# Kernel tuning notes

Measured on AMD Instinct MI355X. Metric: run time of the kernel, lower is better.

The kernel has to match this reference:

```python
import jax, jax.numpy as jnp
import numpy as np

N = 4096      # num_nodes
U = 64        # num_units
IN = 2        # input_dim
DIM = U + IN  # 66
H = 4         # attention heads
ALPHA = 0.2   # leaky slope inside attention scores
SLOPE = 0.01  # nn.LeakyReLU() default for subnet activations
NEG_INF = -9e15


def setup_inputs() -> dict:
    key = jax.random.key(0)
    ks = jax.random.split(key, 20)
    def gn(k, shape, fan):
        return jax.random.normal(k, shape, dtype=jnp.float32) / np.float32(np.sqrt(fan))
    adj = jax.random.randint(ks[2], (N, N), 0, 2, dtype=jnp.int32)
    adj = jnp.maximum(adj, jnp.eye(N, dtype=jnp.int32))  # ensure self-loops
    return {
        "inputs": jax.random.normal(ks[0], (1, N * IN), dtype=jnp.float32),
        "hx": jax.random.normal(ks[1], (1, N, U), dtype=jnp.float32),
        "adj": adj,
        "m1_W": gn(ks[3], (H, DIM, DIM), DIM),
        "m1_a1": gn(ks[4], (H, DIM), DIM),
        "m1_a2": gn(ks[5], (H, DIM), DIM),
        "m1_Wout": gn(ks[6], (H * DIM, DIM), H * DIM),
        "m1_ao1": gn(ks[7], (DIM,), DIM),
        "m1_ao2": gn(ks[8], (DIM,), DIM),
        "m2_W": gn(ks[9], (H, DIM, DIM), DIM),
        "m2_a1": gn(ks[10], (H, DIM), DIM),
        "m2_a2": gn(ks[11], (H, DIM), DIM),
        "m2_Wout": gn(ks[12], (H * DIM, DIM), H * DIM),
        "m2_ao1": gn(ks[13], (DIM,), DIM),
        "m2_ao2": gn(ks[14], (DIM,), DIM),
        "g1_W": gn(ks[15], (DIM, 2 * U), DIM),
        "g1_b": jnp.zeros((2 * U,), dtype=jnp.float32),
        "g2_W": gn(ks[16], (DIM, U), DIM),
        "g2_b": jnp.zeros((U,), dtype=jnp.float32),
    }


def gat_layer(x, W, a1, a2, mask):
    # x: [N,Fin], W: [Fin,Fout], a1/a2: [Fout], mask: [N,N] bool
    h = x @ W                                   # [N,Fout]
    f1 = h @ a1                                 # [N] source term
    f2 = h @ a2                                 # [N] target term
    e = jax.nn.leaky_relu(f1[:, None] + f2[None, :], ALPHA)  # [N,N]
    e = jnp.where(mask, e, NEG_INF)
    attn = jax.nn.softmax(e, axis=-1)
    return attn @ h                             # [N,Fout]


def subnet(x, W, a1, a2, Wout, ao1, ao2, mask):
    # multi-head GAT, concat heads, activation, output GAT layer, activation
    heads = jax.vmap(gat_layer, in_axes=(None, 0, 0, 0, None))(x, W, a1, a2, mask)  # [H,N,DIM]
    hcat = jnp.transpose(heads, (1, 0, 2)).reshape(x.shape[0], -1)                   # [N,H*DIM]
    hcat = jax.nn.leaky_relu(hcat, SLOPE)
    out = gat_layer(hcat, Wout, ao1, ao2, mask)                                      # [N,DIM]
    return jax.nn.leaky_relu(out, SLOPE)


def reference(inputs, hx, adj, m1_W, m1_a1, m1_a2, m1_Wout, m1_ao1, m1_ao2,
              m2_W, m2_a1, m2_a2, m2_Wout, m2_ao1, m2_ao2,
              g1_W, g1_b, g2_W, g2_b):
    mask = adj > 0
    xi = inputs.reshape(N, IN)
    xh = hx.reshape(N, U)
    # _GAT1: concat(inputs, hx) -> GATSubNet1 -> linear -> sigmoid -> split r,u
    x1 = jnp.concatenate([xi, xh], axis=-1)                 # [N,DIM]
    g1 = subnet(x1, m1_W, m1_a1, m1_a2, m1_Wout, m1_ao1, m1_ao2, mask)
    value = jax.nn.sigmoid(g1 @ g1_W + g1_b)                # [N,2U]
    r, u = value[:, :U], value[:, U:]
    # _GAT2: concat(inputs, r*hx) -> GATSubNet2 -> linear -> tanh
    x2 = jnp.concatenate([xi, r * xh], axis=-1)             # [N,DIM]
    g2 = subnet(x2, m2_W, m2_a1, m2_a2, m2_Wout, m2_ao1, m2_ao2, mask)
    c = jnp.tanh(g2 @ g2_W + g2_b)                          # [N,U]
    new_state = u * xh + (1.0 - u) * c
    return new_state.reshape(1, N, U)
```

## Files before the change

### kernel.cpp

```cpp
#include <hip/hip_runtime.h>
#include <hip/hip_bf16.h>

constexpr int kN = 4096;
constexpr int kDim = 66;
constexpr int kH = 4;
constexpr int kU = 64;
constexpr float kAlpha = 0.2f;
constexpr float kSlope = 0.01f;
constexpr float kLog2e = 1.44269504f;

typedef _Float16 half8 __attribute__((ext_vector_type(8)));
typedef _Float16 half2t __attribute__((ext_vector_type(2)));
typedef __attribute__((ext_vector_type(4))) float floatx4;

__device__ inline unsigned int fkey(float f){
  unsigned int u = __float_as_uint(f);
  return (u & 0x80000000u) ? ~u : (u | 0x80000000u);
}
__device__ inline float funkey(unsigned int k){
  unsigned int u = (k & 0x80000000u) ? (k ^ 0x80000000u) : ~k;
  return __uint_as_float(u);
}

__device__ __forceinline__ void gld_lds16(const void* g, void* l){
  __builtin_amdgcn_global_load_lds((const __attribute__((address_space(1))) unsigned int*)g,
                                   (__attribute__((address_space(3))) unsigned int*)l, 16, 0, 0);
}

__global__ void setup_k(const int* __restrict__ adj, unsigned long long* __restrict__ packed,
                        const float* __restrict__ in2, const float* __restrict__ hx,
                        _Float16* __restrict__ x1b, _Float16* __restrict__ x2b,
                        const float* __restrict__ m1W, const float* __restrict__ m1a1, const float* __restrict__ m1a2,
                        const float* __restrict__ m1Wo, const float* __restrict__ m1ao1, const float* __restrict__ m1ao2,
                        const float* __restrict__ m2W, const float* __restrict__ m2a1, const float* __restrict__ m2a2,
                        const float* __restrict__ m2Wo, const float* __restrict__ m2ao1, const float* __restrict__ m2ao2,
                        const float* __restrict__ g1W, const float* __restrict__ g1b,
                        const float* __restrict__ g2W, const float* __restrict__ g2b,
                        _Float16* __restrict__ B1t, _Float16* __restrict__ B1t2,
                        _Float16* __restrict__ B2t, _Float16* __restrict__ B2t2,
                        _Float16* __restrict__ Bgt, _Float16* __restrict__ Bft,
                        unsigned int* __restrict__ fmaxbuf){
  int bb = blockIdx.x, t = threadIdx.x;
  if (bb < 16384){
    int gid = bb * 256 + t;
    unsigned long long m = __ballot(adj[gid] != 0);
    if ((t & 63) == 0) packed[gid >> 6] = m;
    return;
  }
  if (bb < 16384 + 1024){
    int i = (bb - 16384) * 4 + (t >> 6);
    int c = t & 63;
    x1b[(size_t)i * 96 + 2 + c] = (_Float16)hx[(size_t)i * kU + c];
    if (c < 2){
      _Float16 xv = (_Float16)in2[i * 2 + c];
      x1b[(size_t)i * 96 + c] = xv;
      x2b[(size_t)i * 96 + c] = xv;
    }
    if (c < 30){
      x1b[(size_t)i * 96 + 66 + c] = (_Float16)0.f;
      x2b[(size_t)i * 96 + 66 + c] = (_Float16)0.f;
    }
    return;
  }
  int b = bb - (16384 + 1024);
  if (b < 8){
    int m = b & 3;
    const float* W  = (b < 4 ? m1W  : m2W)  + (size_t)m * kDim * kDim;
    const float* a1 = (b < 4 ? m1a1 : m2a1) + m * kDim;
    const float* a2 = (b < 4 ? m1a2 : m2a2) + m * kDim;
    _Float16* Bo = (b < 4 ? B1t : B1t2) + (size_t)m * 80 * 96;
    __shared__ float Ws[kDim * kDim];
    __shared__ float wa1s[kDim], wa2s[kDim];
    for (int z = t; z < kDim * kDim; z += 256) Ws[z] = W[z];
    __syncthreads();
    if (t < kDim){
      float s1 = 0.f, s2 = 0.f;
      for (int d = 0; d < kDim; d++){ float wv = Ws[t * kDim + d]; s1 += wv * a1[d]; s2 += wv * a2[d]; }
      wa1s[t] = s1; wa2s[t] = s2;
    }
    __syncthreads();
    for (int z = t; z < 80 * 96; z += 256){
      int nn = z / 96, k = z % 96;
      float val = 0.f;
      if (k < kDim){
        if (nn < kDim) val = Ws[k * kDim + nn];
        else if (nn == 66) val = wa1s[k];
        else if (nn == 67) val = wa2s[k];
      }
      Bo[z] = (_Float16)val;
    }
  } else if (b < 10){
    const float* Wo  = (b == 8 ? m1Wo  : m2Wo);
    const float* ao1 = (b == 8 ? m1ao1 : m2ao1);
    const float* ao2 = (b == 8 ? m1ao2 : m2ao2);
    _Float16* Bo = (b == 8 ? B2t : B2t2);
    __shared__ float wo1s[264], wo2s[264];
    for (int k = t; k < 264; k += 256){
      float s1 = 0.f, s2 = 0.f;
      for (int d = 0; d < kDim; d++){ float wv = Wo[(size_t)k * kDim + d]; s1 += wv * ao1[d]; s2 += wv * ao2[d]; }
      wo1s[k] = s1; wo2s[k] = s2;
    }
    __syncthreads();
    for (int z = t; z < 80 * 288; z += 256){
      int nn = z / 288, k = z % 288;
      int h = k / 72, c = k - h * 72;
      float val = 0.f;
      if (c < 66){
        int kk = h * 66 + c;
        if (nn < kDim) val = Wo[(size_t)kk * kDim + nn];
        else if (nn == 66) val = wo1s[kk];
        else if (nn == 67) val = wo2s[kk];
      }
      Bo[z] = (_Float16)val;
    }
  } else if (b == 10){
    for (int z = t; z < 128 * 96; z += 256){
      int nn = z / 96, k = z % 96;
      float val = 0.f;
      if (k < kDim) val = g1W[k * 128 + nn];
      else if (k == 66) val = g1b[nn];
      Bgt[z] = (_Float16)val;
    }
  } else {
    if (t < 16) fmaxbuf[t] = 0u;
    for (int z = t; z < 64 * 96; z += 256){
      int nn = z / 96, k = z % 96;
      float val = 0.f;
      if (k < kDim) val = g2W[k * 64 + nn];
      else if (k == 66) val = g2b[nn];
      Bft[z] = (_Float16)val;
    }
  }
}

template<int KSTEPS, int NT, int EPI>
__global__ __launch_bounds__(256) void gemm_k(
    const _Float16* __restrict__ A, const _Float16* __restrict__ Bt,
    void* __restrict__ p0, void* __restrict__ p1, void* __restrict__ p2,
    const float* __restrict__ aux, unsigned int* __restrict__ fmaxp)
{
  constexpr int KP = KSTEPS * 32;
  const int m = blockIdx.y;
  const int i0 = blockIdx.x * 64;
  const int t = threadIdx.x;
  const int w = t >> 6, lane = t & 63, q = lane >> 4, n = lane & 15;
  const int arow = i0 + w * 16 + n;
  const _Float16* Ar = A + (size_t)arow * KP;
  const _Float16* Bm = Bt + (size_t)m * (NT * 16) * KP;
  floatx4 acc[NT];
  #pragma unroll
  for (int v = 0; v < NT; v++) acc[v] = (floatx4){0.f, 0.f, 0.f, 0.f};
  #pragma unroll
  for (int ks = 0; ks < KSTEPS; ks++){
    half8 af = *(const half8*)&Ar[ks * 32 + q * 8];
    #pragma unroll
    for (int nt = 0; nt < NT; nt++){
      half8 bf = *(const half8*)&Bm[(size_t)(nt * 16 + n) * KP + ks * 32 + q * 8];
      acc[nt] = __builtin_amdgcn_mfma_f32_16x16x32_f16(af, bf, acc[nt], 0, 0, 0);
    }
  }
  const int ib = i0 + w * 16 + q * 4;
  if constexpr (EPI == 0){
    _Float16* Ht = (_Float16*)p0 + (size_t)m * 68 * kN;
    float* f1 = (float*)p1 + (size_t)m * kN;
    float* f2 = (float*)p2 + (size_t)m * kN;
    float lm = -3e38f;
    #pragma unroll
    for (int nt = 0; nt < NT; nt++){
      int c = nt * 16 + n;
      if (c < kDim){
        union { _Float16 h[4]; uint2 v; } pk;
        pk.h[0] = (_Float16)acc[nt][0]; pk.h[1] = (_Float16)acc[nt][1];
        pk.h[2] = (_Float16)acc[nt][2]; pk.h[3] = (_Float16)acc[nt][3];
        *(uint2*)&Ht[(size_t)c * kN + ib] = pk.v;
      } else if (c == 66){
        float4 fv; fv.x = acc[nt][0] * kLog2e; fv.y = acc[nt][1] * kLog2e;
        fv.z = acc[nt][2] * kLog2e; fv.w = acc[nt][3] * kLog2e;
        *(float4*)&f1[ib] = fv;
        *(uint2*)&Ht[(size_t)66 * kN + ib] = make_uint2(0x3C003C00u, 0x3C003C00u);
      } else if (c == 67){
        float4 fv; fv.x = acc[nt][0] * kLog2e; fv.y = acc[nt][1] * kLog2e;
        fv.z = acc[nt][2] * kLog2e; fv.w = acc[nt][3] * kLog2e;
        *(float4*)&f2[ib] = fv;
        lm = fmaxf(fmaxf(fv.x, fv.y), fmaxf(fv.z, fv.w));
        *(uint2*)&Ht[(size_t)67 * kN + ib] = make_uint2(0u, 0u);
      }
    }
    lm = fmaxf(lm, __shfl_xor(lm, 16));
    lm = fmaxf(lm, __shfl_xor(lm, 32));
    if (lane == 3) atomicMax(&fmaxp[m], fkey(lm));
  } else if constexpr (EPI == 1){
    float* u = (float*)p0;
    _Float16* x2b = (_Float16*)p1;
    #pragma unroll
    for (int nt = 0; nt < NT; nt++){
      int c = nt * 16 + n;
      #pragma unroll
      for (int r = 0; r < 4; r++){
        float v = 1.f / (1.f + __expf(-acc[nt][r]));
        if (c < 64) x2b[(size_t)(ib + r) * 96 + 2 + c] = (_Float16)(v * aux[(size_t)(ib + r) * kU + c]);
        else        u[(size_t)(ib + r) * kU + (c - 64)] = v;
      }
    }
  } else {
    float* outp = (float*)p0;
    const float* u = (const float*)p1;
    #pragma unroll
    for (int nt = 0; nt < NT; nt++){
      int c = nt * 16 + n;
      #pragma unroll
      for (int r = 0; r < 4; r++){
        float cc = tanhf(acc[nt][r]);
        float uv = u[(size_t)(ib + r) * kU + c];
        outp[(size_t)(ib + r) * kU + c] = uv * aux[(size_t)(ib + r) * kU + c] + (1.f - uv) * cc;
      }
    }
  }
}

template<int JSPLIT>
__global__ __launch_bounds__(256, 4) void attn_mfma_k(
    const _Float16* __restrict__ Ht, const float* __restrict__ f1,
    const float* __restrict__ f2, const unsigned int* __restrict__ fmaxu,
    const unsigned long long* __restrict__ packed,
    _Float16* __restrict__ paccb)
{
  constexpr int JR = kN / JSPLIT;
  constexpr int NCH = JR / 128;
  const int m = blockIdx.y, js = blockIdx.z;
  const int i0 = blockIdx.x * 64;
  const int t = threadIdx.x;
  const int w = t >> 6, lane = t & 63, q = lane >> 4, n = lane & 15;
  const int i = i0 + w * 16 + n;
  const _Float16* Hg = Ht + (size_t)m * 68 * kN;
  const float* f2m = f2 + (size_t)m * kN;
  const float f1v = f1[(size_t)m * kN + i];
  const float fmx = funkey(fmaxu[m]);
  const float t0 = f1v + fmx;
  const float S = fmaxf(t0, kAlpha * t0);
  const float A1f = __builtin_amdgcn_exp2f(t0 - S);
  const float A2f = __builtin_amdgcn_exp2f(kAlpha * t0 - S);
  const half2t a1p = { (_Float16)A1f, (_Float16)A1f };
  const half2t a2p = { (_Float16)A2f, (_Float16)A2f };

  __shared__ __align__(16) _Float16 buf[2][68 * 128];
  __shared__ __align__(16) _Float16 Zro[128];
  __shared__ __align__(16) _Float16 B1h[2][128], B2h[2][128];

  for (int z = t; z < 128; z += 256) Zro[z] = (_Float16)0.f;

  const int r4 = q;
  const int cse = n ^ r4;
  const int cso = cse ^ 4;

  const int jbase = js * JR;
  const unsigned long long* prow = packed + (size_t)i * 64;
  const int jj = (w << 5) | (lane & 31);
  const bool blane = (lane & 32) == 0;

#define STAGE_G(PD, CH) do { \
    const _Float16* gB_ = Hg + jbase + (CH) * 128; \
    _Pragma("unroll") \
    for (int kk_ = 0; kk_ < 5; kk_++){ \
      const int k_ = w + kk_ * 4; \
      if (k_ < 17){ \
        const int row_ = k_ * 4 + r4; \
        const int csw_ = (k_ & 1) ? cso : cse; \
        gld_lds16(gB_ + (size_t)row_ * kN + csw_ * 8, &buf[(PD)][k_ * 512]); \
      } \
    } \
  } while (0)

  floatx4 acc[5];
  #pragma unroll
  for (int v = 0; v < 5; v++) acc[v] = (floatx4){0.f, 0.f, 0.f, 0.f};

  if (blane){
    const float v_ = f2m[jbase + jj] - fmx;
    B1h[0][jj] = (_Float16)__builtin_amdgcn_exp2f(v_);
    B2h[0][jj] = (_Float16)__builtin_amdgcn_exp2f(kAlpha * v_);
  }
  STAGE_G(0, 0);
  __syncthreads();

  int ch = 0;
#define BODY(P) do { \
    const int j0_ = jbase + ch * 128; \
     \
    float f2v_ = 0.f; \
    const bool doB_ = (ch + 1 < NCH) && blane; \
    if (doB_) f2v_ = f2m[j0_ + 128 + jj]; \
    const unsigned long long w0_ = prow[j0_ >> 6]; \
    const unsigned long long w1_ = prow[(j0_ >> 6) + 1]; \
    __builtin_amdgcn_sched_barrier(0); \
    if (ch + 1 < NCH) STAGE_G((P) ^ 1, ch + 1); \
    __builtin_amdgcn_sched_barrier(0); \
    if (doB_){ \
      const float v_ = f2v_ - fmx; \
      B1h[(P) ^ 1][jj] = (_Float16)__builtin_amdgcn_exp2f(v_); \
      B2h[(P) ^ 1][jj] = (_Float16)__builtin_amdgcn_exp2f(kAlpha * v_); \
    } \
    const _Float16* bz_ = (n < 4) ? &buf[(P)][(64 + n) * 128] : Zro; \
    _Pragma("unroll") \
    for (int ks = 0; ks < 4; ks++){ \
      const unsigned long long wsel = (ks < 2) ? w0_ : w1_; \
      const unsigned int bits = (unsigned int)((wsel >> ((ks & 1) * 32 + q * 8)) & 0xffull); \
      union { uint4 v; unsigned int u[4]; } b1v, b2v; \
      b1v.v = *(const uint4*)&B1h[(P)][ks * 32 + q * 8]; \
      b2v.v = *(const uint4*)&B2h[(P)][ks * 32 + q * 8]; \
      union { half8 s; unsigned int u[4]; } af; \
      _Pragma("unroll") \
      for (int e = 0; e < 4; e++){ \
        half2t x1 = __builtin_bit_cast(half2t, b1v.u[e]); \
        half2t x2 = __builtin_bit_cast(half2t, b2v.u[e]); \
        half2t m1 = x1 * a1p; \
        half2t m2 = x2 * a2p; \
        half2t pm = __builtin_elementwise_max(m1, m2); \
        unsigned int mm = (((bits >> (2 * e)) & 1u) ? 0x0000FFFFu : 0u) \
                        | (((bits >> (2 * e + 1)) & 1u) ? 0xFFFF0000u : 0u); \
        af.u[e] = __builtin_bit_cast(unsigned int, pm) & mm; \
      } \
      const int cs_ = ((ks * 4 + q) ^ (n & 7)) * 8; \
      _Pragma("unroll") \
      for (int nt = 0; nt < 4; nt++){ \
        const half8 bf = *(const half8*)&buf[(P)][(nt * 16 + n) * 128 + cs_]; \
        acc[nt] = __builtin_amdgcn_mfma_f32_16x16x32_f16(af.s, bf, acc[nt], 0, 0, 0); \
      } \
      { const half8 bf4 = *(const half8*)&bz_[cs_]; \
        acc[4] = __builtin_amdgcn_mfma_f32_16x16x32_f16(af.s, bf4, acc[4], 0, 0, 0); } \
    } \
    ch++; \
    if (ch < NCH) __syncthreads(); \
  } while (0)

  #pragma unroll 1
  for (int it = 0; it < NCH / 2; it++){
    BODY(0);
    BODY(1);
  }
#undef BODY
#undef STAGE_G

  _Float16* pw = paccb + ((size_t)(m * JSPLIT + js) * kN + (i0 + w * 16)) * 80;
  #pragma unroll
  for (int nt = 0; nt < 5; nt++){
    if (nt < 4 || n < 4){
      #pragma unroll
      for (int r = 0; r < 4; r++)
        pw[(q * 4 + r) * 80 + nt * 16 + n] = (_Float16)acc[nt][r];
    }
  }
}

template<int JSPLIT>
__global__ void combine_k(const _Float16* __restrict__ paccb, _Float16* __restrict__ outb,
                          int ostride, int headoff, int ones_col){
  const int m = blockIdx.y;
  const int t = threadIdx.x;
  const int ri = t >> 2, cg = t & 3;
  const int lane = t & 63;
  const int i = blockIdx.x * 64 + ri;
  const _Float16* pb = paccb + ((size_t)m * JSPLIT * kN + i) * 80;
  float accv[3][8];
  #pragma unroll
  for (int k = 0; k < 3; k++)
    #pragma unroll
    for (int e = 0; e < 8; e++) accv[k][e] = 0.f;
  #pragma unroll
  for (int s = 0; s < JSPLIT; s++){
    const _Float16* ps = pb + (size_t)s * kN * 80;
    #pragma unroll
    for (int k = 0; k < 3; k++){
      const int c = cg + 4 * k;
      if (c < 9){
        union { uint4 v; _Float16 h[8]; } uu;
        uu.v = *(const uint4*)&ps[c * 8];
        #pragma unroll
        for (int e = 0; e < 8; e++) accv[k][e] += (float)uu.h[e];
      }
    }
  }
  float l = accv[2][2];
  l = __shfl(l, lane & ~3, 64);
  const float inv = 1.f / l;
  _Float16* orow = outb + (size_t)i * ostride + m * headoff;
  #pragma unroll
  for (int k = 0; k < 3; k++){
    const int c = cg + 4 * k;
    if (c < 9){
      union { uint4 v; _Float16 h[8]; } uu;
      #pragma unroll
      for (int e = 0; e < 8; e++){
        float v = accv[k][e] * inv;
        v = fmaxf(v, kSlope * v);
        uu.h[e] = (_Float16)v;
      }
      if (c == 8){
        uu.h[2] = (_Float16)(ones_col ? 1.f : 0.f);
        #pragma unroll
        for (int e = 3; e < 8; e++) uu.h[e] = (_Float16)0.f;
      }
      *(uint4*)&orow[c * 8] = uu.v;
    }
  }
}

extern "C" void kernel_launch(void* const* d_in, const int* in_sizes, int n_in,
                              void* d_out, int out_size, void* d_ws, size_t ws_size,
                              hipStream_t stream){
  const float* inputs  = (const float*)d_in[0];
  const float* hx      = (const float*)d_in[1];
  const int*   adj     = (const int*)d_in[2];
  const float* m1_W    = (const float*)d_in[3];
  const float* m1_a1   = (const float*)d_in[4];
  const float* m1_a2   = (const float*)d_in[5];
  const float* m1_Wout = (const float*)d_in[6];
  const float* m1_ao1  = (const float*)d_in[7];
  const float* m1_ao2  = (const float*)d_in[8];
  const float* m2_W    = (const float*)d_in[9];
  const float* m2_a1   = (const float*)d_in[10];
  const float* m2_a2   = (const float*)d_in[11];
  const float* m2_Wout = (const float*)d_in[12];
  const float* m2_ao1  = (const float*)d_in[13];
  const float* m2_ao2  = (const float*)d_in[14];
  const float* g1_W    = (const float*)d_in[15];
  const float* g1_b    = (const float*)d_in[16];
  const float* g2_W    = (const float*)d_in[17];
  const float* g2_b    = (const float*)d_in[18];
  float* out = (float*)d_out;

  char* ws = (char*)d_ws;
  size_t off = 0;
  auto alloc = [&](size_t bytes) -> void* {
    void* p = ws + off;
    off = (off + bytes + 255) & ~(size_t)255;
    return p;
  };
  unsigned long long* packed = (unsigned long long*)alloc((size_t)kN * 64 * 8);
  _Float16* x1b  = (_Float16*)alloc((size_t)kN * 96 * 2);
  _Float16* x2b  = (_Float16*)alloc((size_t)kN * 96 * 2);
  _Float16* Ht   = (_Float16*)alloc((size_t)kH * 68 * kN * 2);
  _Float16* Hto  = (_Float16*)alloc((size_t)68 * kN * 2);
  _Float16* hcatb= (_Float16*)alloc((size_t)kN * 288 * 2);
  _Float16* gb   = (_Float16*)alloc((size_t)kN * 96 * 2);
  _Float16* g2bv = (_Float16*)alloc((size_t)kN * 96 * 2);
  float* f1   = (float*)alloc((size_t)kH * kN * 4);
  float* f2   = (float*)alloc((size_t)kH * kN * 4);
  float* fo1  = (float*)alloc((size_t)kN * 4);
  float* fo2  = (float*)alloc((size_t)kN * 4);
  unsigned int* fmaxbuf = (unsigned int*)alloc(64);
  float* u    = (float*)alloc((size_t)kN * kU * 4);
  _Float16* paccb = (_Float16*)alloc((size_t)16 * kN * 80 * 2);
  _Float16* B1t  = (_Float16*)alloc((size_t)kH * 80 * 96 * 2);
  _Float16* B1t2 = (_Float16*)alloc((size_t)kH * 80 * 96 * 2);
  _Float16* B2t  = (_Float16*)alloc((size_t)80 * 288 * 2);
  _Float16* B2t2 = (_Float16*)alloc((size_t)80 * 288 * 2);
  _Float16* Bgt  = (_Float16*)alloc((size_t)128 * 96 * 2);
  _Float16* Bft  = (_Float16*)alloc((size_t)64 * 96 * 2);
  (void)ws_size; (void)in_sizes; (void)n_in; (void)out_size;

  setup_k<<<16384 + 1024 + 12, 256, 0, stream>>>(adj, packed, inputs, hx, x1b, x2b,
      m1_W, m1_a1, m1_a2, m1_Wout, m1_ao1, m1_ao2,
      m2_W, m2_a1, m2_a2, m2_Wout, m2_ao1, m2_ao2,
      g1_W, g1_b, g2_W, g2_b,
      B1t, B1t2, B2t, B2t2, Bgt, Bft, fmaxbuf);

  gemm_k<3, 5, 0><<<dim3(64, kH), 256, 0, stream>>>(x1b, B1t, Ht, f1, f2, nullptr, fmaxbuf + 0);
  attn_mfma_k<4><<<dim3(64, kH, 4), 256, 0, stream>>>(Ht, f1, f2, fmaxbuf + 0, packed, paccb);
  combine_k<4><<<dim3(64, kH), 256, 0, stream>>>(paccb, hcatb, 288, 72, 0);
  gemm_k<9, 5, 0><<<dim3(64, 1), 256, 0, stream>>>(hcatb, B2t, Hto, fo1, fo2, nullptr, fmaxbuf + 4);
  attn_mfma_k<8><<<dim3(64, 1, 8), 256, 0, stream>>>(Hto, fo1, fo2, fmaxbuf + 4, packed, paccb);
  combine_k<8><<<dim3(64, 1), 256, 0, stream>>>(paccb, gb, 96, 0, 1);
  gemm_k<3, 8, 1><<<dim3(64, 1), 256, 0, stream>>>(gb, Bgt, u, x2b, nullptr, hx, nullptr);

  gemm_k<3, 5, 0><<<dim3(64, kH), 256, 0, stream>>>(x2b, B1t2, Ht, f1, f2, nullptr, fmaxbuf + 5);
  attn_mfma_k<4><<<dim3(64, kH, 4), 256, 0, stream>>>(Ht, f1, f2, fmaxbuf + 5, packed, paccb);
  combine_k<4><<<dim3(64, kH), 256, 0, stream>>>(paccb, hcatb, 288, 72, 0);
  gemm_k<9, 5, 0><<<dim3(64, 1), 256, 0, stream>>>(hcatb, B2t2, Hto, fo1, fo2, nullptr, fmaxbuf + 9);
  attn_mfma_k<8><<<dim3(64, 1, 8), 256, 0, stream>>>(Hto, fo1, fo2, fmaxbuf + 9, packed, paccb);
  combine_k<8><<<dim3(64, 1), 256, 0, stream>>>(paccb, g2bv, 96, 0, 1);
  gemm_k<3, 4, 2><<<dim3(64, 1), 256, 0, stream>>>(g2bv, Bft, out, u, nullptr, hx, nullptr);
}
```

Baseline: 293.8 us.

## Fuse split-K combine into following GEMM and double rows per attention block

The separate combine kernels are removed: the GEMM that follows each attention pass now reduces the split partial accumulators itself, normalises them, applies the activation into shared memory, and then runs the MFMA GEMM from LDS. The attention kernel now processes 128 rows per block (two 64-row sets) and reuses each staged H tile and exp tables for both, with launch bounds lowered to 2 blocks per CU. The output attention layer uses 16 j-splits instead of 8. This cuts launches and global round trips and halves the LDS staging traffic per row, in exchange for more registers and lower occupancy in attention, and more partial-sum reads in the fused combine.

New measurement: 313.0 us. 1.07x slower.

```diff
diff --git a/kernel.cpp b/kernel.cpp
--- a/kernel.cpp
+++ b/kernel.cpp
@@ -133,11 +133,11 @@
   }
 }
 
-template<int KSTEPS, int NT, int EPI>
+template<int KSTEPS, int NT>
 __global__ __launch_bounds__(256) void gemm_k(
     const _Float16* __restrict__ A, const _Float16* __restrict__ Bt,
     void* __restrict__ p0, void* __restrict__ p1, void* __restrict__ p2,
-    const float* __restrict__ aux, unsigned int* __restrict__ fmaxp)
+    unsigned int* __restrict__ fmaxp)
 {
   constexpr int KP = KSTEPS * 32;
   const int m = blockIdx.y;
@@ -146,6 +146,116 @@
   const int w = t >> 6, lane = t & 63, q = lane >> 4, n = lane & 15;
   const int arow = i0 + w * 16 + n;
   const _Float16* Ar = A + (size_t)arow * KP;
+  const _Float16* Bm = Bt + (size_t)m * (NT * 16) * KP;
+  floatx4 acc[NT];
+  #pragma unroll
+  for (int v = 0; v < NT; v++) acc[v] = (floatx4){0.f, 0.f, 0.f, 0.f};
+  #pragma unroll
+  for (int ks = 0; ks < KSTEPS; ks++){
+    half8 af = *(const half8*)&Ar[ks * 32 + q * 8];
+    #pragma unroll
+    for (int nt = 0; nt < NT; nt++){
+      half8 bf = *(const half8*)&Bm[(size_t)(nt * 16 + n) * KP + ks * 32 + q * 8];
+      acc[nt] = __builtin_amdgcn_mfma_f32_16x16x32_f16(af, bf, acc[nt], 0, 0, 0);
+    }
+  }
+  const int ib = i0 + w * 16 + q * 4;
+  _Float16* Ht = (_Float16*)p0 + (size_t)m * 68 * kN;
+  float* f1 = (float*)p1 + (size_t)m * kN;
+  float* f2 = (float*)p2 + (size_t)m * kN;
+  float lm = -3e38f;
+  #pragma unroll
+  for (int nt = 0; nt < NT; nt++){
+    int c = nt * 16 + n;
+    if (c < kDim){
+      union { _Float16 h[4]; uint2 v; } pk;
+      pk.h[0] = (_Float16)acc[nt][0]; pk.h[1] = (_Float16)acc[nt][1];
+      pk.h[2] = (_Float16)acc[nt][2]; pk.h[3] = (_Float16)acc[nt][3];
+      *(uint2*)&Ht[(size_t)c * kN + ib] = pk.v;
+    } else if (c == 66){
+      float4 fv; fv.x = acc[nt][0] * kLog2e; fv.y = acc[nt][1] * kLog2e;
+      fv.z = acc[nt][2] * kLog2e; fv.w = acc[nt][3] * kLog2e;
+      *(float4*)&f1[ib] = fv;
+      *(uint2*)&Ht[(size_t)66 * kN + ib] = make_uint2(0x3C003C00u, 0x3C003C00u);
+    } else if (c == 67){
+      float4 fv; fv.x = acc[nt][0] * kLog2e; fv.y = acc[nt][1] * kLog2e;
+      fv.z = acc[nt][2] * kLog2e; fv.w = acc[nt][3] * kLog2e;
+      *(float4*)&f2[ib] = fv;
+      lm = fmaxf(fmaxf(fv.x, fv.y), fmaxf(fv.z, fv.w));
+      *(uint2*)&Ht[(size_t)67 * kN + ib] = make_uint2(0u, 0u);
+    }
+  }
+  lm = fmaxf(lm, __shfl_xor(lm, 16));
+  lm = fmaxf(lm, __shfl_xor(lm, 32));
+  if (lane == 3) atomicMax(&fmaxp[m], fkey(lm));
+}
+
+template<int SPLITS, int HEADS, int KSTEPS, int NT, int EPI, int LDK, int ONES>
+__global__ __launch_bounds__(256) void gemm_comb_k(
+    const _Float16* __restrict__ pacc, const _Float16* __restrict__ Bt,
+    void* __restrict__ p0, void* __restrict__ p1, void* __restrict__ p2,
+    const float* __restrict__ aux, unsigned int* __restrict__ fmaxp)
+{
+  constexpr int KP = KSTEPS * 32;
+  __shared__ __align__(16) _Float16 Asm[64 * LDK];
+  const int i0 = blockIdx.x * 64;
+  const int t = threadIdx.x;
+  {
+    const int ri = t >> 2, cg = t & 3, ln = t & 63;
+    const int row = i0 + ri;
+    #pragma unroll
+    for (int h = 0; h < HEADS; h++){
+      const _Float16* pb = pacc + ((size_t)h * SPLITS * kN + row) * 80;
+      float accv[3][8];
+      #pragma unroll
+      for (int k = 0; k < 3; k++)
+        #pragma unroll
+        for (int e = 0; e < 8; e++) accv[k][e] = 0.f;
+      #pragma unroll
+      for (int s = 0; s < SPLITS; s++){
+        const _Float16* ps = pb + (size_t)s * kN * 80;
+        #pragma unroll
+        for (int k = 0; k < 3; k++){
+          const int c = cg + 4 * k;
+          if (c < 9){
+            union { uint4 v; _Float16 h8[8]; } uu;
+            uu.v = *(const uint4*)&ps[c * 8];
+            #pragma unroll
+            for (int e = 0; e < 8; e++) accv[k][e] += (float)uu.h8[e];
+          }
+        }
+      }
+      float l = accv[2][2];
+      l = __shfl(l, ln & ~3, 64);
+      const float inv = 1.f / l;
+      #pragma unroll
+      for (int k = 0; k < 3; k++){
+        const int c = cg + 4 * k;
+        union { uint4 v; _Float16 h8[8]; } uu;
+        if (c < 9){
+          #pragma unroll
+          for (int e = 0; e < 8; e++){
+            float v = accv[k][e] * inv;
+            v = fmaxf(v, kSlope * v);
+            uu.h8[e] = (_Float16)v;
+          }
+          if (c == 8){
+            uu.h8[2] = (_Float16)(ONES ? 1.f : 0.f);
+            #pragma unroll
+            for (int e = 3; e < 8; e++) uu.h8[e] = (_Float16)0.f;
+          }
+          *(uint4*)&Asm[(size_t)ri * LDK + h * 72 + c * 8] = uu.v;
+        } else if (HEADS == 1 && c < 12){
+          uu.v = make_uint4(0u, 0u, 0u, 0u);
+          *(uint4*)&Asm[(size_t)ri * LDK + c * 8] = uu.v;
+        }
+      }
+    }
+  }
+  __syncthreads();
+  const int m = blockIdx.y;
+  const int w = t >> 6, lane = t & 63, q = lane >> 4, n = lane & 15;
+  const _Float16* Ar = &Asm[(size_t)(w * 16 + n) * LDK];
   const _Float16* Bm = Bt + (size_t)m * (NT * 16) * KP;
   floatx4 acc[NT];
   #pragma unroll
@@ -219,7 +329,7 @@
 }
 
 template<int JSPLIT>
-__global__ __launch_bounds__(256, 4) void attn_mfma_k(
+__global__ __launch_bounds__(256, 2) void attn_mfma_k(
     const _Float16* __restrict__ Ht, const float* __restrict__ f1,
     const float* __restrict__ f2, const unsigned int* __restrict__ fmaxu,
     const unsigned long long* __restrict__ packed,
@@ -228,20 +338,23 @@
   constexpr int JR = kN / JSPLIT;
   constexpr int NCH = JR / 128;
   const int m = blockIdx.y, js = blockIdx.z;
-  const int i0 = blockIdx.x * 64;
+  const int i0 = blockIdx.x * 128;
   const int t = threadIdx.x;
   const int w = t >> 6, lane = t & 63, q = lane >> 4, n = lane & 15;
-  const int i = i0 + w * 16 + n;
+  const int ia = i0 + w * 16 + n;
   const _Float16* Hg = Ht + (size_t)m * 68 * kN;
   const float* f2m = f2 + (size_t)m * kN;
-  const float f1v = f1[(size_t)m * kN + i];
   const float fmx = funkey(fmaxu[m]);
-  const float t0 = f1v + fmx;
-  const float S = fmaxf(t0, kAlpha * t0);
-  const float A1f = __builtin_amdgcn_exp2f(t0 - S);
-  const float A2f = __builtin_amdgcn_exp2f(kAlpha * t0 - S);
-  const half2t a1p = { (_Float16)A1f, (_Float16)A1f };
-  const half2t a2p = { (_Float16)A2f, (_Float16)A2f };
+  const float t0a = f1[(size_t)m * kN + ia] + fmx;
+  const float t0b = f1[(size_t)m * kN + ia + 64] + fmx;
+  const float Sa = fmaxf(t0a, kAlpha * t0a);
+  const float Sb = fmaxf(t0b, kAlpha * t0b);
+  const _Float16 A1a = (_Float16)__builtin_amdgcn_exp2f(t0a - Sa);
+  const _Float16 A2a = (_Float16)__builtin_amdgcn_exp2f(kAlpha * t0a - Sa);
+  const _Float16 A1b = (_Float16)__builtin_amdgcn_exp2f(t0b - Sb);
+  const _Float16 A2b = (_Float16)__builtin_amdgcn_exp2f(kAlpha * t0b - Sb);
+  const half2t a1pa = { A1a, A1a }, a2pa = { A2a, A2a };
+  const half2t a1pb = { A1b, A1b }, a2pb = { A2b, A2b };
 
   __shared__ __align__(16) _Float16 buf[2][68 * 128];
   __shared__ __align__(16) _Float16 Zro[128];
@@ -254,7 +367,8 @@
   const int cso = cse ^ 4;
 
   const int jbase = js * JR;
-  const unsigned long long* prow = packed + (size_t)i * 64;
+  const unsigned long long* prA = packed + (size_t)ia * 64;
+  const unsigned long long* prB = prA + 64ll * 64;
   const int jj = (w << 5) | (lane & 31);
   const bool blane = (lane & 32) == 0;
 
@@ -271,9 +385,12 @@
     } \
   } while (0)
 
-  floatx4 acc[5];
-  #pragma unroll
-  for (int v = 0; v < 5; v++) acc[v] = (floatx4){0.f, 0.f, 0.f, 0.f};
+  floatx4 acca[5], accb[5];
+  #pragma unroll
+  for (int v = 0; v < 5; v++){
+    acca[v] = (floatx4){0.f, 0.f, 0.f, 0.f};
+    accb[v] = (floatx4){0.f, 0.f, 0.f, 0.f};
+  }
 
   if (blane){
     const float v_ = f2m[jbase + jj] - fmx;
@@ -286,12 +403,13 @@
   int ch = 0;
 #define BODY(P) do { \
     const int j0_ = jbase + ch * 128; \
-     \
     float f2v_ = 0.f; \
     const bool doB_ = (ch + 1 < NCH) && blane; \
     if (doB_) f2v_ = f2m[j0_ + 128 + jj]; \
-    const unsigned long long w0_ = prow[j0_ >> 6]; \
-    const unsigned long long w1_ = prow[(j0_ >> 6) + 1]; \
+    const unsigned long long w0a_ = prA[j0_ >> 6]; \
+    const unsigned long long w1a_ = prA[(j0_ >> 6) + 1]; \
+    const unsigned long long w0b_ = prB[j0_ >> 6]; \
+    const unsigned long long w1b_ = prB[(j0_ >> 6) + 1]; \
     __builtin_amdgcn_sched_barrier(0); \
     if (ch + 1 < NCH) STAGE_G((P) ^ 1, ch + 1); \
     __builtin_amdgcn_sched_barrier(0); \
@@ -303,31 +421,36 @@
     const _Float16* bz_ = (n < 4) ? &buf[(P)][(64 + n) * 128] : Zro; \
     _Pragma("unroll") \
     for (int ks = 0; ks < 4; ks++){ \
-      const unsigned long long wsel = (ks < 2) ? w0_ : w1_; \
-      const unsigned int bits = (unsigned int)((wsel >> ((ks & 1) * 32 + q * 8)) & 0xffull); \
+      const int sh_ = (ks & 1) * 32 + q * 8; \
+      const unsigned int ba_ = (unsigned int)((((ks < 2) ? w0a_ : w1a_) >> sh_) & 0xffull); \
+      const unsigned int bb_ = (unsigned int)((((ks < 2) ? w0b_ : w1b_) >> sh_) & 0xffull); \
       union { uint4 v; unsigned int u[4]; } b1v, b2v; \
       b1v.v = *(const uint4*)&B1h[(P)][ks * 32 + q * 8]; \
       b2v.v = *(const uint4*)&B2h[(P)][ks * 32 + q * 8]; \
-      union { half8 s; unsigned int u[4]; } af; \
+      union { half8 s; unsigned int u[4]; } afa, afb; \
       _Pragma("unroll") \
       for (int e = 0; e < 4; e++){ \
         half2t x1 = __builtin_bit_cast(half2t, b1v.u[e]); \
         half2t x2 = __builtin_bit_cast(half2t, b2v.u[e]); \
-        half2t m1 = x1 * a1p; \
-        half2t m2 = x2 * a2p; \
-        half2t pm = __builtin_elementwise_max(m1, m2); \
-        unsigned int mm = (((bits >> (2 * e)) & 1u) ? 0x0000FFFFu : 0u) \
-                        | (((bits >> (2 * e + 1)) & 1u) ? 0xFFFF0000u : 0u); \
-        af.u[e] = __builtin_bit_cast(unsigned int, pm) & mm; \
+        half2t pa = __builtin_elementwise_max(x1 * a1pa, x2 * a2pa); \
+        half2t pb = __builtin_elementwise_max(x1 * a1pb, x2 * a2pb); \
+        unsigned int ma = (((ba_ >> (2 * e)) & 1u) ? 0x0000FFFFu : 0u) \
+                        | (((ba_ >> (2 * e + 1)) & 1u) ? 0xFFFF0000u : 0u); \
+        unsigned int mb = (((bb_ >> (2 * e)) & 1u) ? 0x0000FFFFu : 0u) \
+                        | (((bb_ >> (2 * e + 1)) & 1u) ? 0xFFFF0000u : 0u); \
+        afa.u[e] = __builtin_bit_cast(unsigned int, pa) & ma; \
+        afb.u[e] = __builtin_bit_cast(unsigned int, pb) & mb; \
       } \
       const int cs_ = ((ks * 4 + q) ^ (n & 7)) * 8; \
       _Pragma("unroll") \
       for (int nt = 0; nt < 4; nt++){ \
         const half8 bf = *(const half8*)&buf[(P)][(nt * 16 + n) * 128 + cs_]; \
-        acc[nt] = __builtin_amdgcn_mfma_f32_16x16x32_f16(af.s, bf, acc[nt], 0, 0, 0); \
+        acca[nt] = __builtin_amdgcn_mfma_f32_16x16x32_f16(afa.s, bf, acca[nt], 0, 0, 0); \
+        accb[nt] = __builtin_amdgcn_mfma_f32_16x16x32_f16(afb.s, bf, accb[nt], 0, 0, 0); \
       } \
       { const half8 bf4 = *(const half8*)&bz_[cs_]; \
-        acc[4] = __builtin_amdgcn_mfma_f32_16x16x32_f16(af.s, bf4, acc[4], 0, 0, 0); } \
+        acca[4] = __builtin_amdgcn_mfma_f32_16x16x32_f16(afa.s, bf4, acca[4], 0, 0, 0); \
+        accb[4] = __builtin_amdgcn_mfma_f32_16x16x32_f16(afb.s, bf4, accb[4], 0, 0, 0); } \
     } \
     ch++; \
     if (ch < NCH) __syncthreads(); \
@@ -341,66 +464,16 @@
 #undef BODY
 #undef STAGE_G
 
-  _Float16* pw = paccb + ((size_t)(m * JSPLIT + js) * kN + (i0 + w * 16)) * 80;
+  _Float16* pwa = paccb + ((size_t)(m * JSPLIT + js) * kN + (i0 + w * 16)) * 80;
+  _Float16* pwb = pwa + (size_t)64 * 80;
   #pragma unroll
   for (int nt = 0; nt < 5; nt++){
     if (nt < 4 || n < 4){
       #pragma unroll
-      for (int r = 0; r < 4; r++)
-        pw[(q * 4 + r) * 80 + nt * 16 + n] = (_Float16)acc[nt][r];
-    }
-  }
-}
-
-template<int JSPLIT>
-__global__ void combine_k(const _Float16* __restrict__ paccb, _Float16* __restrict__ outb,
-                          int ostride, int headoff, int ones_col){
-  const int m = blockIdx.y;
-  const int t = threadIdx.x;
-  const int ri = t >> 2, cg = t & 3;
-  const int lane = t & 63;
-  const int i = blockIdx.x * 64 + ri;
-  const _Float16* pb = paccb + ((size_t)m * JSPLIT * kN + i) * 80;
-  float accv[3][8];
-  #pragma unroll
-  for (int k = 0; k < 3; k++)
-    #pragma unroll
-    for (int e = 0; e < 8; e++) accv[k][e] = 0.f;
-  #pragma unroll
-  for (int s = 0; s < JSPLIT; s++){
-    const _Float16* ps = pb + (size_t)s * kN * 80;
-    #pragma unroll
-    for (int k = 0; k < 3; k++){
-      const int c = cg + 4 * k;
-      if (c < 9){
-        union { uint4 v; _Float16 h[8]; } uu;
-        uu.v = *(const uint4*)&ps[c * 8];
-        #pragma unroll
-        for (int e = 0; e < 8; e++) accv[k][e] += (float)uu.h[e];
-      }
-    }
-  }
-  float l = accv[2][2];
-  l = __shfl(l, lane & ~3, 64);
-  const float inv = 1.f / l;
-  _Float16* orow = outb + (size_t)i * ostride + m * headoff;
-  #pragma unroll
-  for (int k = 0; k < 3; k++){
-    const int c = cg + 4 * k;
-    if (c < 9){
-      union { uint4 v; _Float16 h[8]; } uu;
-      #pragma unroll
-      for (int e = 0; e < 8; e++){
-        float v = accv[k][e] * inv;
-        v = fmaxf(v, kSlope * v);
-        uu.h[e] = (_Float16)v;
-      }
-      if (c == 8){
-        uu.h[2] = (_Float16)(ones_col ? 1.f : 0.f);
-        #pragma unroll
-        for (int e = 3; e < 8; e++) uu.h[e] = (_Float16)0.f;
-      }
-      *(uint4*)&orow[c * 8] = uu.v;
+      for (int r = 0; r < 4; r++){
+        pwa[(q * 4 + r) * 80 + nt * 16 + n] = (_Float16)acca[nt][r];
+        pwb[(q * 4 + r) * 80 + nt * 16 + n] = (_Float16)accb[nt][r];
+      }
     }
   }
 }
@@ -441,9 +514,6 @@
   _Float16* x2b  = (_Float16*)alloc((size_t)kN * 96 * 2);
   _Float16* Ht   = (_Float16*)alloc((size_t)kH * 68 * kN * 2);
   _Float16* Hto  = (_Float16*)alloc((size_t)68 * kN * 2);
-  _Float16* hcatb= (_Float16*)alloc((size_t)kN * 288 * 2);
-  _Float16* gb   = (_Float16*)alloc((size_t)kN * 96 * 2);
-  _Float16* g2bv = (_Float16*)alloc((size_t)kN * 96 * 2);
   float* f1   = (float*)alloc((size_t)kH * kN * 4);
   float* f2   = (float*)alloc((size_t)kH * kN * 4);
   float* fo1  = (float*)alloc((size_t)kN * 4);
@@ -465,19 +535,15 @@
       g1_W, g1_b, g2_W, g2_b,
       B1t, B1t2, B2t, B2t2, Bgt, Bft, fmaxbuf);
 
-  gemm_k<3, 5, 0><<<dim3(64, kH), 256, 0, stream>>>(x1b, B1t, Ht, f1, f2, nullptr, fmaxbuf + 0);
-  attn_mfma_k<4><<<dim3(64, kH, 4), 256, 0, stream>>>(Ht, f1, f2, fmaxbuf + 0, packed, paccb);
-  combine_k<4><<<dim3(64, kH), 256, 0, stream>>>(paccb, hcatb, 288, 72, 0);
-  gemm_k<9, 5, 0><<<dim3(64, 1), 256, 0, stream>>>(hcatb, B2t, Hto, fo1, fo2, nullptr, fmaxbuf + 4);
-  attn_mfma_k<8><<<dim3(64, 1, 8), 256, 0, stream>>>(Hto, fo1, fo2, fmaxbuf + 4, packed, paccb);
-  combine_k<8><<<dim3(64, 1), 256, 0, stream>>>(paccb, gb, 96, 0, 1);
-  gemm_k<3, 8, 1><<<dim3(64, 1), 256, 0, stream>>>(gb, Bgt, u, x2b, nullptr, hx, nullptr);
-
-  gemm_k<3, 5, 0><<<dim3(64, kH), 256, 0, stream>>>(x2b, B1t2, Ht, f1, f2, nullptr, fmaxbuf + 5);
-  attn_mfma_k<4><<<dim3(64, kH, 4), 256, 0, stream>>>(Ht, f1, f2, fmaxbuf + 5, packed, paccb);
-  combine_k<4><<<dim3(64, kH), 256, 0, stream>>>(paccb, hcatb, 288, 72, 0);
-  gemm_k<9, 5, 0><<<dim3(64, 1), 256, 0, stream>>>(hcatb, B2t2, Hto, fo1, fo2, nullptr, fmaxbuf + 9);
-  attn_mfma_k<8><<<dim3(64, 1, 8), 256, 0, stream>>>(Hto, fo1, fo2, fmaxbuf + 9, packed, paccb);
-  combine_k<8><<<dim3(64, 1), 256, 0, stream>>>(paccb, g2bv, 96, 0, 1);
-  gemm_k<3, 4, 2><<<dim3(64, 1), 256, 0, stream>>>(g2bv, Bft, out, u, nullptr, hx, nullptr);
-}
+  gemm_k<3, 5><<<dim3(64, kH), 256, 0, stream>>>(x1b, B1t, Ht, f1, f2, fmaxbuf + 0);
+  attn_mfma_k<4><<<dim3(32, kH, 4), 256, 0, stream>>>(Ht, f1, f2, fmaxbuf + 0, packed, paccb);
+  gemm_comb_k<4, 4, 9, 5, 0, 296, 0><<<dim3(64, 1), 256, 0, stream>>>(paccb, B2t, Hto, fo1, fo2, nullptr, fmaxbuf + 4);
+  attn_mfma_k<16><<<dim3(32, 1, 16), 256, 0, stream>>>(Hto, fo1, fo2, fmaxbuf + 4, packed, paccb);
+  gemm_comb_k<16, 1, 3, 8, 1, 104, 1><<<dim3(64, 1), 256, 0, stream>>>(paccb, Bgt, u, x2b, nullptr, hx, nullptr);
+
+  gemm_k<3, 5><<<dim3(64, kH), 256, 0, stream>>>(x2b, B1t2, Ht, f1, f2, fmaxbuf + 5);
+  attn_mfma_k<4><<<dim3(32, kH, 4), 256, 0, stream>>>(Ht, f1, f2, fmaxbuf + 5, packed, paccb);
+  gemm_comb_k<4, 4, 9, 5, 0, 296, 0><<<dim3(64, 1), 256, 0, stream>>>(paccb, B2t2, Hto, fo1, fo2, nullptr, fmaxbuf + 9);
+  attn_mfma_k<16><<<dim3(32, 1, 16), 256, 0, stream>>>(Hto, fo1, fo2, fmaxbuf + 9, packed, paccb);
+  gemm_comb_k<16, 1, 3, 4, 2, 104, 1><<<dim3(64, 1), 256, 0, stream>>>(paccb, Bft, out, u, nullptr, hx, nullptr);
+}
```

## Increase grid parallelism: single-wave gemm blocks, wider combine, 16-way j-split on output attention

Applied to the files above, without the earlier changes.

Each gemm block now runs one 64-thread wave covering 16 rows, so every gemm launches four times as many blocks. The output-layer attention splits the neighbour dimension 16 ways instead of 8. The combine kernel gives each thread a single 8-column slice, with 8 threads per row and 32 rows per block. The aim is to fill more compute units in these small kernels, at the cost of twice the partial-accumulator traffic that combine must read for the output layer.

Result: slower. 305.9 us (+4.1%).

```diff
diff --git a/kernel.cpp b/kernel.cpp
--- a/kernel.cpp
+++ b/kernel.cpp
@@ -134,17 +134,17 @@
 }
 
 template<int KSTEPS, int NT, int EPI>
-__global__ __launch_bounds__(256) void gemm_k(
+__global__ __launch_bounds__(64) void gemm_k(
     const _Float16* __restrict__ A, const _Float16* __restrict__ Bt,
     void* __restrict__ p0, void* __restrict__ p1, void* __restrict__ p2,
     const float* __restrict__ aux, unsigned int* __restrict__ fmaxp)
 {
   constexpr int KP = KSTEPS * 32;
   const int m = blockIdx.y;
-  const int i0 = blockIdx.x * 64;
-  const int t = threadIdx.x;
-  const int w = t >> 6, lane = t & 63, q = lane >> 4, n = lane & 15;
-  const int arow = i0 + w * 16 + n;
+  const int i0 = blockIdx.x * 16;
+  const int lane = threadIdx.x;
+  const int q = lane >> 4, n = lane & 15;
+  const int arow = i0 + n;
   const _Float16* Ar = A + (size_t)arow * KP;
   const _Float16* Bm = Bt + (size_t)m * (NT * 16) * KP;
   floatx4 acc[NT];
@@ -159,7 +159,7 @@
       acc[nt] = __builtin_amdgcn_mfma_f32_16x16x32_f16(af, bf, acc[nt], 0, 0, 0);
     }
   }
-  const int ib = i0 + w * 16 + q * 4;
+  const int ib = i0 + q * 4;
   if constexpr (EPI == 0){
     _Float16* Ht = (_Float16*)p0 + (size_t)m * 68 * kN;
     float* f1 = (float*)p1 + (size_t)m * kN;
@@ -286,7 +286,6 @@
   int ch = 0;
 #define BODY(P) do { \
     const int j0_ = jbase + ch * 128; \
-     \
     float f2v_ = 0.f; \
     const bool doB_ = (ch + 1 < NCH) && blane; \
     if (doB_) f2v_ = f2m[j0_ + 128 + jj]; \
@@ -353,55 +352,59 @@
 }
 
 template<int JSPLIT>
-__global__ void combine_k(const _Float16* __restrict__ paccb, _Float16* __restrict__ outb,
+__global__ __launch_bounds__(256) void combine_k(const _Float16* __restrict__ paccb,
+                          _Float16* __restrict__ outb,
                           int ostride, int headoff, int ones_col){
   const int m = blockIdx.y;
   const int t = threadIdx.x;
-  const int ri = t >> 2, cg = t & 3;
+  const int ri = t >> 3, cg = t & 7;
   const int lane = t & 63;
-  const int i = blockIdx.x * 64 + ri;
+  const int i = blockIdx.x * 32 + ri;
   const _Float16* pb = paccb + ((size_t)m * JSPLIT * kN + i) * 80;
-  float accv[3][8];
-  #pragma unroll
-  for (int k = 0; k < 3; k++)
+  float accv[2][8];
+  #pragma unroll
+  for (int k = 0; k < 2; k++)
     #pragma unroll
     for (int e = 0; e < 8; e++) accv[k][e] = 0.f;
   #pragma unroll
   for (int s = 0; s < JSPLIT; s++){
     const _Float16* ps = pb + (size_t)s * kN * 80;
-    #pragma unroll
-    for (int k = 0; k < 3; k++){
-      const int c = cg + 4 * k;
-      if (c < 9){
-        union { uint4 v; _Float16 h[8]; } uu;
-        uu.v = *(const uint4*)&ps[c * 8];
-        #pragma unroll
-        for (int e = 0; e < 8; e++) accv[k][e] += (float)uu.h[e];
-      }
-    }
-  }
-  float l = accv[2][2];
-  l = __shfl(l, lane & ~3, 64);
+    union { uint4 v; _Float16 h[8]; } uu;
+    uu.v = *(const uint4*)&ps[cg * 8];
+    #pragma unroll
+    for (int e = 0; e < 8; e++) accv[0][e] += (float)uu.h[e];
+    if (cg == 0){
+      uu.v = *(const uint4*)&ps[64];
+      #pragma unroll
+      for (int e = 0; e < 8; e++) accv[1][e] += (float)uu.h[e];
+    }
+  }
+  float l = accv[1][2];
+  l = __shfl(l, lane & 56, 64);
   const float inv = 1.f / l;
   _Float16* orow = outb + (size_t)i * ostride + m * headoff;
-  #pragma unroll
-  for (int k = 0; k < 3; k++){
-    const int c = cg + 4 * k;
-    if (c < 9){
-      union { uint4 v; _Float16 h[8]; } uu;
-      #pragma unroll
-      for (int e = 0; e < 8; e++){
-        float v = accv[k][e] * inv;
-        v = fmaxf(v, kSlope * v);
-        uu.h[e] = (_Float16)v;
-      }
-      if (c == 8){
-        uu.h[2] = (_Float16)(ones_col ? 1.f : 0.f);
-        #pragma unroll
-        for (int e = 3; e < 8; e++) uu.h[e] = (_Float16)0.f;
-      }
-      *(uint4*)&orow[c * 8] = uu.v;
-    }
+  {
+    union { uint4 v; _Float16 h[8]; } uu;
+    #pragma unroll
+    for (int e = 0; e < 8; e++){
+      float v = accv[0][e] * inv;
+      v = fmaxf(v, kSlope * v);
+      uu.h[e] = (_Float16)v;
+    }
+    *(uint4*)&orow[cg * 8] = uu.v;
+  }
+  if (cg == 0){
+    union { uint4 v; _Float16 h[8]; } uu;
+    #pragma unroll
+    for (int e = 0; e < 2; e++){
+      float v = accv[1][e] * inv;
+      v = fmaxf(v, kSlope * v);
+      uu.h[e] = (_Float16)v;
+    }
+    uu.h[2] = (_Float16)(ones_col ? 1.f : 0.f);
+    #pragma unroll
+    for (int e = 3; e < 8; e++) uu.h[e] = (_Float16)0.f;
+    *(uint4*)&orow[64] = uu.v;
   }
 }
 
@@ -465,19 +468,19 @@
       g1_W, g1_b, g2_W, g2_b,
       B1t, B1t2, B2t, B2t2, Bgt, Bft, fmaxbuf);
 
-  gemm_k<3, 5, 0><<<dim3(64, kH), 256, 0, stream>>>(x1b, B1t, Ht, f1, f2, nullptr, fmaxbuf + 0);
+  gemm_k<3, 5, 0><<<dim3(256, kH), 64, 0, stream>>>(x1b, B1t, Ht, f1, f2, nullptr, fmaxbuf + 0);
   attn_mfma_k<4><<<dim3(64, kH, 4), 256, 0, stream>>>(Ht, f1, f2, fmaxbuf + 0, packed, paccb);
-  combine_k<4><<<dim3(64, kH), 256, 0, stream>>>(paccb, hcatb, 288, 72, 0);
-  gemm_k<9, 5, 0><<<dim3(64, 1), 256, 0, stream>>>(hcatb, B2t, Hto, fo1, fo2, nullptr, fmaxbuf + 4);
-  attn_mfma_k<8><<<dim3(64, 1, 8), 256, 0, stream>>>(Hto, fo1, fo2, fmaxbuf + 4, packed, paccb);
-  combine_k<8><<<dim3(64, 1), 256, 0, stream>>>(paccb, gb, 96, 0, 1);
-  gemm_k<3, 8, 1><<<dim3(64, 1), 256, 0, stream>>>(gb, Bgt, u, x2b, nullptr, hx, nullptr);
-
-  gemm_k<3, 5, 0><<<dim3(64, kH), 256, 0, stream>>>(x2b, B1t2, Ht, f1, f2, nullptr, fmaxbuf + 5);
+  combine_k<4><<<dim3(128, kH), 256, 0, stream>>>(paccb, hcatb, 288, 72, 0);
+  gemm_k<9, 5, 0><<<dim3(256, 1), 64, 0, stream>>>(hcatb, B2t, Hto, fo1, fo2, nullptr, fmaxbuf + 4);
+  attn_mfma_k<16><<<dim3(64, 1, 16), 256, 0, stream>>>(Hto, fo1, fo2, fmaxbuf + 4, packed, paccb);
+  combine_k<16><<<dim3(128, 1), 256, 0, stream>>>(paccb, gb, 96, 0, 1);
+  gemm_k<3, 8, 1><<<dim3(256, 1), 64, 0, stream>>>(gb, Bgt, u, x2b, nullptr, hx, nullptr);
+
+  gemm_k<3, 5, 0><<<dim3(256, kH), 64, 0, stream>>>(x2b, B1t2, Ht, f1, f2, nullptr, fmaxbuf + 5);
   attn_mfma_k<4><<<dim3(64, kH, 4), 256, 0, stream>>>(Ht, f1, f2, fmaxbuf + 5, packed, paccb);
-  combine_k<4><<<dim3(64, kH), 256, 0, stream>>>(paccb, hcatb, 288, 72, 0);
-  gemm_k<9, 5, 0><<<dim3(64, 1), 256, 0, stream>>>(hcatb, B2t2, Hto, fo1, fo2, nullptr, fmaxbuf + 9);
-  attn_mfma_k<8><<<dim3(64, 1, 8), 256, 0, stream>>>(Hto, fo1, fo2, fmaxbuf + 9, packed, paccb);
-  combine_k<8><<<dim3(64, 1), 256, 0, stream>>>(paccb, g2bv, 96, 0, 1);
-  gemm_k<3, 4, 2><<<dim3(64, 1), 256, 0, stream>>>(g2bv, Bft, out, u, nullptr, hx, nullptr);
-}
+  combine_k<4><<<dim3(128, kH), 256, 0, stream>>>(paccb, hcatb, 288, 72, 0);
+  gemm_k<9, 5, 0><<<dim3(256, 1), 64, 0, stream>>>(hcatb, B2t2, Hto, fo1, fo2, nullptr, fmaxbuf + 9);
+  attn_mfma_k<16><<<dim3(64, 1, 16), 256, 0, stream>>>(Hto, fo1, fo2, fmaxbuf + 9, packed, paccb);
+  combine_k<16><<<dim3(128, 1), 256, 0, stream>>>(paccb, g2bv, 96, 0, 1);
+  gemm_k<3, 4, 2><<<dim3(256, 1), 64, 0, stream>>>(g2bv, Bft, out, u, nullptr, hx, nullptr);
+}
```
